# Kernel tuning notes

Measured on AMD Instinct MI355X. Metric: run time of the kernel, lower is better.

Reference implementation:

```python
import jax, jax.numpy as jnp
import numpy as np
import math

B, S, KV_DIM, Q_DIM, E, H = 16, 8192, 512, 512, 512, 8
D = E // H  # head_dim = 64


def setup_inputs() -> dict:
    key = jax.random.key(0)
    ks = jax.random.split(key, 12)
    s_q = 1.0 / math.sqrt(Q_DIM)
    s_kv = 1.0 / math.sqrt(KV_DIM)
    s_e = 1.0 / math.sqrt(E)
    return {
        "query": jax.random.normal(ks[0], (B, Q_DIM), dtype=jnp.float32),
        "key_value": jax.random.normal(ks[1], (B, S, KV_DIM), dtype=jnp.float32),
        "Wq": jax.random.uniform(ks[2], (Q_DIM, E), jnp.float32, -s_q, s_q),
        "bq": jax.random.uniform(ks[3], (E,), jnp.float32, -s_q, s_q),
        "Wk": jax.random.uniform(ks[4], (KV_DIM, E), jnp.float32, -s_kv, s_kv),
        "bk": jax.random.uniform(ks[5], (E,), jnp.float32, -s_kv, s_kv),
        "Wv": jax.random.uniform(ks[6], (KV_DIM, E), jnp.float32, -s_kv, s_kv),
        "bv": jax.random.uniform(ks[7], (E,), jnp.float32, -s_kv, s_kv),
        "Wo": jax.random.uniform(ks[8], (E, E), jnp.float32, -s_e, s_e),
        "bo": jax.random.uniform(ks[9], (E,), jnp.float32, -s_e, s_e),
    }


def reference(query, key_value, Wq, bq, Wk, bk, Wv, bv, Wo, bo):
    bsz, seq_len, _ = key_value.shape
    # q: [B, H, D] (single query per batch)
    q = (query @ Wq + bq).reshape(bsz, H, D)
    # k, v: [B, S, H, D]
    k = (key_value @ Wk + bk).reshape(bsz, seq_len, H, D)
    v = (key_value @ Wv + bv).reshape(bsz, seq_len, H, D)
    scale = 1.0 / math.sqrt(D)
    # attn logits: [B, H, S]
    attn = jnp.einsum("bhd,bshd->bhs", q, k) * scale
    weights = jax.nn.softmax(attn, axis=-1)
    # context: [B, H, D] -> [B, E]
    context = jnp.einsum("bhs,bshd->bhd", weights, v).reshape(bsz, E)
    return context @ Wo + bo
```

## Files before the change

### kernel.cpp

```cpp
#include <hip/hip_runtime.h>
#include <math.h>

#define B_   16
#define S_   8192
#define KVD  512
#define E_   512
#define H_   8
#define D_   64

__global__ __launch_bounds__(256) void k_fold(const float* __restrict__ query,
                                              const float* __restrict__ Wq,
                                              const float* __restrict__ bq,
                                              const float* __restrict__ Wk,
                                              float* __restrict__ qk_vec) {
    const int b = blockIdx.y, cc = blockIdx.x;
    const int tid = threadIdx.x;
    __shared__ float qs[E_];

    const float* qrow = query + (size_t)b * 512;
    #pragma unroll
    for (int i = 0; i < 2; ++i) {
        int e = tid + i * 256;
        float a0 = bq[e], a1 = 0.f, a2 = 0.f, a3 = 0.f;
        for (int k = 0; k < 512; k += 4) {
            a0 = fmaf(qrow[k],     Wq[(size_t)(k)     * E_ + e], a0);
            a1 = fmaf(qrow[k + 1], Wq[(size_t)(k + 1) * E_ + e], a1);
            a2 = fmaf(qrow[k + 2], Wq[(size_t)(k + 2) * E_ + e], a2);
            a3 = fmaf(qrow[k + 3], Wq[(size_t)(k + 3) * E_ + e], a3);
        }
        qs[e] = ((a0 + a1) + (a2 + a3)) * 0.125f;
    }
    __syncthreads();

    #pragma unroll
    for (int i = 0; i < 2; ++i) {
        int idx = tid + i * 256;
        int c = cc * 64 + (idx & 63);
        int h = idx >> 6;
        const float* wkr = Wk + (size_t)c * E_ + h * D_;
        const float* qh  = qs + h * D_;
        float a0 = 0.f, a1 = 0.f, a2 = 0.f, a3 = 0.f;
        #pragma unroll
        for (int d = 0; d < D_; d += 4) {
            a0 = fmaf(qh[d],     wkr[d],     a0);
            a1 = fmaf(qh[d + 1], wkr[d + 1], a1);
            a2 = fmaf(qh[d + 2], wkr[d + 2], a2);
            a3 = fmaf(qh[d + 3], wkr[d + 3], a3);
        }
        qk_vec[((size_t)b * H_ + h) * KVD + c] = (a0 + a1) + (a2 + a3);
    }
}

template <int NC>
__global__ __launch_bounds__(256, 2) void k_attn(const float* __restrict__ kv,
                                                 const float* __restrict__ qk_vec,
                                                 float* __restrict__ pctx,
                                                 float* __restrict__ pml) {
    constexpr int CHUNK = S_ / NC;
    constexpr int RPW = CHUNK / 4;
    constexpr int RB = 4;
    constexpr int NIT = RPW / RB;
    constexpr int SROW = 68;
    constexpr int SPW = RB * H_ * SROW;

    __shared__ __align__(16) float scr[4 * SPW];
    __shared__ __align__(16) float wb[4][RB * H_];
    __shared__ __align__(16) float ab[4][H_];
    __shared__ __align__(16) float mW[4][H_];
    __shared__ __align__(16) float lW[4][H_];
    __shared__ __align__(16) float cbuf[H_][KVD];

    const int tid = threadIdx.x;
    const int lane = tid & 63;
    const int w = tid >> 6;
    const int b = blockIdx.y, nc = blockIdx.x;
    const int hme = lane >> 3;
    const int seg = lane & 7;

    float qk[H_][8];
    {
        const float* qb = qk_vec + (size_t)b * H_ * KVD;
        #pragma unroll
        for (int h = 0; h < H_; ++h) {
            float4 v0 = *(const float4*)&qb[h * KVD + lane * 4];
            float4 v1 = *(const float4*)&qb[h * KVD + 256 + lane * 4];
            qk[h][0] = v0.x; qk[h][1] = v0.y; qk[h][2] = v0.z; qk[h][3] = v0.w;
            qk[h][4] = v1.x; qk[h][5] = v1.y; qk[h][6] = v1.z; qk[h][7] = v1.w;
        }
    }

    float ctx[H_][8];
    #pragma unroll
    for (int h = 0; h < H_; ++h)
        #pragma unroll
        for (int j = 0; j < 8; ++j) ctx[h][j] = 0.f;

    float m_run = -INFINITY, l_run = 0.f;

    float* wscr = scr + w * SPW;
    const float* rdb = wscr + hme * SROW + seg * 8;
    const float* kvbase = kv + ((size_t)b * S_ + (size_t)nc * CHUNK + (size_t)w * RPW) * KVD;

    #pragma unroll 1
    for (int it = 0; it < NIT; ++it) {
        float kvr[RB][8];
        #pragma unroll
        for (int r = 0; r < RB; ++r) {
            const float* rowp = kvbase + (size_t)(it * RB + r) * KVD;
            float4 v0 = *(const float4*)&rowp[lane * 4];
            float4 v1 = *(const float4*)&rowp[256 + lane * 4];
            kvr[r][0] = v0.x; kvr[r][1] = v0.y; kvr[r][2] = v0.z; kvr[r][3] = v0.w;
            kvr[r][4] = v1.x; kvr[r][5] = v1.y; kvr[r][6] = v1.z; kvr[r][7] = v1.w;
        }

        #pragma unroll
        for (int r = 0; r < RB; ++r) {
            #pragma unroll
            for (int h = 0; h < H_; ++h) {
                float p = 0.f;
                #pragma unroll
                for (int j = 0; j < 8; ++j) p = fmaf(kvr[r][j], qk[h][j], p);
                wscr[(r * H_ + h) * SROW + lane] = p;
            }
        }

        float lg[RB];
        #pragma unroll
        for (int r = 0; r < RB; ++r) {
            const float* p = rdb + r * H_ * SROW;
            float4 x = *(const float4*)p;
            float4 y = *(const float4*)(p + 4);
            float s = ((x.x + x.y) + (x.z + x.w)) + ((y.x + y.y) + (y.z + y.w));
            s += __shfl_xor(s, 1);
            s += __shfl_xor(s, 2);
            s += __shfl_xor(s, 4);
            lg[r] = s;
        }

        float bmax = lg[0];
        #pragma unroll
        for (int r = 1; r < RB; ++r) bmax = fmaxf(bmax, lg[r]);
        float nm = fmaxf(m_run, bmax);
        float alpha = __expf(m_run - nm);
        m_run = nm;
        float wj[RB], sw = 0.f;
        #pragma unroll
        for (int r = 0; r < RB; ++r) { wj[r] = __expf(lg[r] - nm); sw += wj[r]; }
        l_run = fmaf(l_run, alpha, sw);

        if (seg == 0) {
            #pragma unroll
            for (int r = 0; r < RB; ++r) wb[w][r * H_ + hme] = wj[r];
            ab[w][hme] = alpha;
        }
        float4 A0 = *(const float4*)&ab[w][0];
        float4 A1 = *(const float4*)&ab[w][4];
        float al[8] = {A0.x, A0.y, A0.z, A0.w, A1.x, A1.y, A1.z, A1.w};
        #pragma unroll
        for (int h = 0; h < H_; ++h)
            #pragma unroll
            for (int j = 0; j < 8; ++j) ctx[h][j] *= al[h];

        #pragma unroll
        for (int r = 0; r < RB; ++r) {
            float4 W0 = *(const float4*)&wb[w][r * H_];
            float4 W1 = *(const float4*)&wb[w][r * H_ + 4];
            float wv[8] = {W0.x, W0.y, W0.z, W0.w, W1.x, W1.y, W1.z, W1.w};
            #pragma unroll
            for (int h = 0; h < H_; ++h)
                #pragma unroll
                for (int j = 0; j < 8; ++j)
                    ctx[h][j] = fmaf(wv[h], kvr[r][j], ctx[h][j]);
        }
    }

    if (seg == 0) { mW[w][hme] = m_run; lW[w][hme] = l_run; }
    __syncthreads();

    float Mh[H_];
    #pragma unroll
    for (int h = 0; h < H_; ++h)
        Mh[h] = fmaxf(fmaxf(mW[0][h], mW[1][h]), fmaxf(mW[2][h], mW[3][h]));

    if (w == 0) {
        #pragma unroll
        for (int h = 0; h < H_; ++h) {
            float f = __expf(mW[0][h] - Mh[h]);
            #pragma unroll
            for (int j = 0; j < 8; ++j) ctx[h][j] *= f;
        }
    }
    #pragma unroll 1
    for (int src = 1; src < 4; ++src) {
        if (w == src) {
            #pragma unroll
            for (int h = 0; h < H_; ++h) {
                *(float4*)&cbuf[h][lane * 4]       = make_float4(ctx[h][0], ctx[h][1], ctx[h][2], ctx[h][3]);
                *(float4*)&cbuf[h][256 + lane * 4] = make_float4(ctx[h][4], ctx[h][5], ctx[h][6], ctx[h][7]);
            }
        }
        __syncthreads();
        if (w == 0) {
            #pragma unroll
            for (int h = 0; h < H_; ++h) {
                float f = __expf(mW[src][h] - Mh[h]);
                float4 c0 = *(const float4*)&cbuf[h][lane * 4];
                float4 c1 = *(const float4*)&cbuf[h][256 + lane * 4];
                ctx[h][0] = fmaf(f, c0.x, ctx[h][0]);
                ctx[h][1] = fmaf(f, c0.y, ctx[h][1]);
                ctx[h][2] = fmaf(f, c0.z, ctx[h][2]);
                ctx[h][3] = fmaf(f, c0.w, ctx[h][3]);
                ctx[h][4] = fmaf(f, c1.x, ctx[h][4]);
                ctx[h][5] = fmaf(f, c1.y, ctx[h][5]);
                ctx[h][6] = fmaf(f, c1.z, ctx[h][6]);
                ctx[h][7] = fmaf(f, c1.w, ctx[h][7]);
            }
        }
        __syncthreads();
    }

    if (w == 0) {
        size_t base = (((size_t)b * NC + nc) * H_) * KVD;
        #pragma unroll
        for (int h = 0; h < H_; ++h) {
            *(float4*)&pctx[base + h * KVD + lane * 4] =
                make_float4(ctx[h][0], ctx[h][1], ctx[h][2], ctx[h][3]);
            *(float4*)&pctx[base + h * KVD + 256 + lane * 4] =
                make_float4(ctx[h][4], ctx[h][5], ctx[h][6], ctx[h][7]);
        }
    }
    if (tid < H_) {
        float M = fmaxf(fmaxf(mW[0][tid], mW[1][tid]), fmaxf(mW[2][tid], mW[3][tid]));
        float L = 0.f;
        #pragma unroll
        for (int ww = 0; ww < 4; ++ww) L += __expf(mW[ww][tid] - M) * lW[ww][tid];
        size_t mlidx = ((size_t)b * NC + nc) * H_ + tid;
        pml[mlidx * 2]     = M;
        pml[mlidx * 2 + 1] = L;
    }
}

template <int NC>
__global__ __launch_bounds__(256) void k_combine(const float* __restrict__ pctx,
                                                 const float* __restrict__ pml,
                                                 float* __restrict__ ctx_kv) {
    int bh = blockIdx.x;
    int b = bh >> 3, h = bh & 7;
    int tid = threadIdx.x;

    float mstar = -INFINITY;
    for (int nc = 0; nc < NC; ++nc)
        mstar = fmaxf(mstar, pml[(((size_t)b * NC + nc) * H_ + h) * 2]);

    float lsum = 0.f, acc0 = 0.f, acc1 = 0.f;
    int c = tid * 2;
    for (int nc = 0; nc < NC; ++nc) {
        size_t mlidx = ((size_t)b * NC + nc) * H_ + h;
        float m = pml[mlidx * 2], l = pml[mlidx * 2 + 1];
        float f = __expf(m - mstar);
        lsum = fmaf(l, f, lsum);
        float2 v = *(const float2*)&pctx[(((size_t)b * NC + nc) * H_ + h) * KVD + c];
        acc0 = fmaf(f, v.x, acc0);
        acc1 = fmaf(f, v.y, acc1);
    }
    float inv = 1.0f / lsum;
    *(float2*)&ctx_kv[((size_t)b * H_ + h) * KVD + c] = make_float2(acc0 * inv, acc1 * inv);
}

__global__ __launch_bounds__(512) void k_out(const float* __restrict__ ctx_kv,
                                             const float* __restrict__ Wv,
                                             const float* __restrict__ bv,
                                             const float* __restrict__ Wo,
                                             const float* __restrict__ bo,
                                             float* __restrict__ out) {
    const int b = blockIdx.y, ec = blockIdx.x;
    const int tid = threadIdx.x;
    __shared__ float ctxs[E_];
    __shared__ float psum[4][128];

    {
        int e = tid, h = e >> 6;
        const float* ck = ctx_kv + ((size_t)b * H_ + h) * KVD;
        float a0 = bv[e], a1 = 0.f, a2 = 0.f, a3 = 0.f;
        for (int c = 0; c < KVD; c += 4) {
            a0 = fmaf(ck[c],     Wv[(size_t)(c)     * E_ + e], a0);
            a1 = fmaf(ck[c + 1], Wv[(size_t)(c + 1) * E_ + e], a1);
            a2 = fmaf(ck[c + 2], Wv[(size_t)(c + 2) * E_ + e], a2);
            a3 = fmaf(ck[c + 3], Wv[(size_t)(c + 3) * E_ + e], a3);
        }
        ctxs[e] = (a0 + a1) + (a2 + a3);
    }
    __syncthreads();
    {
        int el = tid & 127, q = tid >> 7;
        int e = ec * 128 + el;
        const float* cs = ctxs + q * 128;
        const float* wo = Wo + (size_t)q * 128 * E_ + e;
        float a0 = 0.f, a1 = 0.f, a2 = 0.f, a3 = 0.f;
        for (int k = 0; k < 128; k += 4) {
            a0 = fmaf(cs[k],     wo[(size_t)(k)     * E_], a0);
            a1 = fmaf(cs[k + 1], wo[(size_t)(k + 1) * E_], a1);
            a2 = fmaf(cs[k + 2], wo[(size_t)(k + 2) * E_], a2);
            a3 = fmaf(cs[k + 3], wo[(size_t)(k + 3) * E_], a3);
        }
        psum[q][el] = (a0 + a1) + (a2 + a3);
    }
    __syncthreads();
    if (tid < 128) {
        int e = ec * 128 + tid;
        out[(size_t)b * E_ + e] =
            bo[e] + ((psum[0][tid] + psum[1][tid]) + (psum[2][tid] + psum[3][tid]));
    }
}

extern "C" void kernel_launch(void* const* d_in, const int* in_sizes, int n_in,
                              void* d_out, int out_size, void* d_ws, size_t ws_size,
                              hipStream_t stream) {
    const float* query = (const float*)d_in[0];
    const float* kv    = (const float*)d_in[1];
    const float* Wq    = (const float*)d_in[2];
    const float* bq    = (const float*)d_in[3];
    const float* Wk    = (const float*)d_in[4];
    const float* Wv    = (const float*)d_in[6];
    const float* bv    = (const float*)d_in[7];
    const float* Wo    = (const float*)d_in[8];
    const float* bo    = (const float*)d_in[9];
    float* out = (float*)d_out;
    float* wsf = (float*)d_ws;

    auto need_bytes = [](size_t nc) {
        return (131072ull + nc * (65536ull + 256ull)) * 4ull;
    };

    float* qk_vec = wsf;
    k_fold<<<dim3(8, B_), 256, 0, stream>>>(query, Wq, bq, Wk, qk_vec);

    if (ws_size >= need_bytes(64)) {
        constexpr int NC = 64;
        float* pctx   = wsf + 65536;
        float* pml    = pctx + (size_t)NC * 65536;
        float* ctx_kv = pml + (size_t)NC * 256;
        k_attn<NC><<<dim3(NC, B_), 256, 0, stream>>>(kv, qk_vec, pctx, pml);
        k_combine<NC><<<B_ * H_, 256, 0, stream>>>(pctx, pml, ctx_kv);
        k_out<<<dim3(4, B_), 512, 0, stream>>>(ctx_kv, Wv, bv, Wo, bo, out);
    } else if (ws_size >= need_bytes(32)) {
        constexpr int NC = 32;
        float* pctx   = wsf + 65536;
        float* pml    = pctx + (size_t)NC * 65536;
        float* ctx_kv = pml + (size_t)NC * 256;
        k_attn<NC><<<dim3(NC, B_), 256, 0, stream>>>(kv, qk_vec, pctx, pml);
        k_combine<NC><<<B_ * H_, 256, 0, stream>>>(pctx, pml, ctx_kv);
        k_out<<<dim3(4, B_), 512, 0, stream>>>(ctx_kv, Wv, bv, Wo, bo, out);
    } else {
        constexpr int NC = 16;
        float* pctx   = wsf + 65536;
        float* pml    = pctx + (size_t)NC * 65536;
        float* ctx_kv = pml + (size_t)NC * 256;
        k_attn<NC><<<dim3(NC, B_), 256, 0, stream>>>(kv, qk_vec, pctx, pml);
        k_combine<NC><<<B_ * H_, 256, 0, stream>>>(pctx, pml, ctx_kv);
        k_out<<<dim3(4, B_), 512, 0, stream>>>(ctx_kv, Wv, bv, Wo, bo, out);
    }
}
```

Baseline: 467.1 us.

## Drop softmax max tracking, double-buffer KV loads, and atomically reduce partials

The attention loop drops the running-max online softmax. It exponentiates raw logits, passes weights across lanes with shuffles instead of shared memory, and double-buffers the KV row loads in registers. The per-chunk partial buffers and the combine kernel are replaced by shared and global atomic accumulation into zeroed workspace. The small projections are split into more blocks that also finish with atomics. Together these cut ALU work, syncs and launch overhead, but exp without max subtraction can overflow for large logits, and the atomic accumulation makes the result nondeterministic.

After: 488.2 us. +4.5%, slower.

```diff
diff --git a/kernel.cpp b/kernel.cpp
--- a/kernel.cpp
+++ b/kernel.cpp
@@ -8,74 +8,163 @@
 #define H_   8
 #define D_   64
 
-__global__ __launch_bounds__(256) void k_fold(const float* __restrict__ query,
-                                              const float* __restrict__ Wq,
+#define OFF_QKVEC   0
+#define OFF_QBUF    65536
+#define OFF_LACC    73728
+#define OFF_CTXACC  73856
+#define OFF_CTXBUF  139392
+#define WS_FLOATS   147584
+#define ZERO_START  OFF_QBUF
+#define ZERO_COUNT  82048
+
+__global__ __launch_bounds__(256) void k_init(float* __restrict__ wsf,
+                                              float* __restrict__ out) {
+    int i = blockIdx.x * 256 + threadIdx.x;
+    const int nws4 = ZERO_COUNT / 4;
+    if (i < nws4) {
+        *(float4*)&wsf[ZERO_START + i * 4] = make_float4(0.f, 0.f, 0.f, 0.f);
+    } else if (i < nws4 + (B_ * E_) / 4) {
+        *(float4*)&out[(i - nws4) * 4] = make_float4(0.f, 0.f, 0.f, 0.f);
+    }
+}
+
+__global__ __launch_bounds__(512) void k_q(const float* __restrict__ query,
+                                           const float* __restrict__ Wq,
+                                           float* __restrict__ q_buf) {
+    const int kc = blockIdx.x, b = blockIdx.y;
+    const int e = threadIdx.x;
+    __shared__ float qs[128];
+    if (e < 128) qs[e] = query[(size_t)b * 512 + kc * 128 + e];
+    __syncthreads();
+    const float* wq = Wq + (size_t)(kc * 128) * E_ + e;
+    float a0 = 0.f, a1 = 0.f, a2 = 0.f, a3 = 0.f;
+    for (int k = 0; k < 128; k += 4) {
+        a0 = fmaf(qs[k],     wq[(size_t)(k)     * E_], a0);
+        a1 = fmaf(qs[k + 1], wq[(size_t)(k + 1) * E_], a1);
+        a2 = fmaf(qs[k + 2], wq[(size_t)(k + 2) * E_], a2);
+        a3 = fmaf(qs[k + 3], wq[(size_t)(k + 3) * E_], a3);
+    }
+    atomicAdd(&q_buf[(size_t)b * E_ + e], (a0 + a1) + (a2 + a3));
+}
+
+__global__ __launch_bounds__(256) void k_fold(const float* __restrict__ q_buf,
                                               const float* __restrict__ bq,
                                               const float* __restrict__ Wk,
                                               float* __restrict__ qk_vec) {
-    const int b = blockIdx.y, cc = blockIdx.x;
+    const int cc = blockIdx.x, h = blockIdx.y;
     const int tid = threadIdx.x;
-    __shared__ float qs[E_];
-
-    const float* qrow = query + (size_t)b * 512;
-    #pragma unroll
-    for (int i = 0; i < 2; ++i) {
-        int e = tid + i * 256;
-        float a0 = bq[e], a1 = 0.f, a2 = 0.f, a3 = 0.f;
-        for (int k = 0; k < 512; k += 4) {
-            a0 = fmaf(qrow[k],     Wq[(size_t)(k)     * E_ + e], a0);
-            a1 = fmaf(qrow[k + 1], Wq[(size_t)(k + 1) * E_ + e], a1);
-            a2 = fmaf(qrow[k + 2], Wq[(size_t)(k + 2) * E_ + e], a2);
-            a3 = fmaf(qrow[k + 3], Wq[(size_t)(k + 3) * E_ + e], a3);
-        }
-        qs[e] = ((a0 + a1) + (a2 + a3)) * 0.125f;
-    }
-    __syncthreads();
-
-    #pragma unroll
-    for (int i = 0; i < 2; ++i) {
-        int idx = tid + i * 256;
-        int c = cc * 64 + (idx & 63);
-        int h = idx >> 6;
-        const float* wkr = Wk + (size_t)c * E_ + h * D_;
-        const float* qh  = qs + h * D_;
-        float a0 = 0.f, a1 = 0.f, a2 = 0.f, a3 = 0.f;
-        #pragma unroll
-        for (int d = 0; d < D_; d += 4) {
-            a0 = fmaf(qh[d],     wkr[d],     a0);
-            a1 = fmaf(qh[d + 1], wkr[d + 1], a1);
-            a2 = fmaf(qh[d + 2], wkr[d + 2], a2);
-            a3 = fmaf(qh[d + 3], wkr[d + 3], a3);
-        }
-        qk_vec[((size_t)b * H_ + h) * KVD + c] = (a0 + a1) + (a2 + a3);
-    }
+    const int c0 = cc * 64;
+    __shared__ float wk[64 * 65];
+    __shared__ float qh[16 * 64];
+
+    #pragma unroll
+    for (int k = 0; k < 4; ++k) {
+        int f4i = tid + k * 256;
+        int row = f4i >> 4, d4 = f4i & 15;
+        float4 v = *(const float4*)&Wk[(size_t)(c0 + row) * E_ + h * D_ + d4 * 4];
+        wk[row * 65 + d4 * 4 + 0] = v.x;
+        wk[row * 65 + d4 * 4 + 1] = v.y;
+        wk[row * 65 + d4 * 4 + 2] = v.z;
+        wk[row * 65 + d4 * 4 + 3] = v.w;
+    }
+    #pragma unroll
+    for (int k = 0; k < 4; ++k) {
+        int idx = tid + k * 256;
+        int b = idx >> 6, d = idx & 63;
+        qh[idx] = (q_buf[(size_t)b * E_ + h * D_ + d] + bq[h * D_ + d]) * 0.125f;
+    }
+    __syncthreads();
+
+    const int c_local = tid & 63, w = tid >> 6;
+    float acc[4] = {0.f, 0.f, 0.f, 0.f};
+    for (int d = 0; d < 64; ++d) {
+        float wv = wk[c_local * 65 + d];
+        #pragma unroll
+        for (int i = 0; i < 4; ++i)
+            acc[i] = fmaf(qh[(w * 4 + i) * 64 + d], wv, acc[i]);
+    }
+    #pragma unroll
+    for (int i = 0; i < 4; ++i) {
+        int b = w * 4 + i;
+        qk_vec[((size_t)b * H_ + h) * KVD + c0 + c_local] = acc[i];
+    }
+}
+
+#define SROW 68
+#define RB   4
+
+template <int NC>
+__device__ __forceinline__ void attn_loadrows(float (&kvr)[RB][8],
+                                              const float* __restrict__ base,
+                                              int it, int lane) {
+    #pragma unroll
+    for (int r = 0; r < RB; ++r) {
+        const float* rowp = base + (size_t)(it * RB + r) * KVD;
+        float4 v0 = *(const float4*)&rowp[lane * 4];
+        float4 v1 = *(const float4*)&rowp[256 + lane * 4];
+        kvr[r][0] = v0.x; kvr[r][1] = v0.y; kvr[r][2] = v0.z; kvr[r][3] = v0.w;
+        kvr[r][4] = v1.x; kvr[r][5] = v1.y; kvr[r][6] = v1.z; kvr[r][7] = v1.w;
+    }
+}
+
+__device__ __forceinline__ void attn_process(const float (&kvr)[RB][8],
+                                             const float (&qk)[H_][8],
+                                             float (&ctx)[H_][8], float& l_run,
+                                             float* __restrict__ wscr,
+                                             const float* __restrict__ rdb,
+                                             int lane) {
+    const int seg = lane & 7;
+    #pragma unroll
+    for (int r = 0; r < RB; ++r)
+        #pragma unroll
+        for (int h = 0; h < H_; ++h) {
+            float p = 0.f;
+            #pragma unroll
+            for (int j = 0; j < 8; ++j) p = fmaf(kvr[r][j], qk[h][j], p);
+            wscr[(r * H_ + h) * SROW + lane] = p;
+        }
+    float e4[RB];
+    #pragma unroll
+    for (int r = 0; r < RB; ++r) {
+        const float* p = rdb + r * H_ * SROW;
+        float4 x = *(const float4*)p;
+        float4 y = *(const float4*)(p + 4);
+        float s = ((x.x + x.y) + (x.z + x.w)) + ((y.x + y.y) + (y.z + y.w));
+        s += __shfl_xor(s, 1);
+        s += __shfl_xor(s, 2);
+        s += __shfl_xor(s, 4);
+        e4[r] = __expf(s);
+        l_run += e4[r];
+    }
+    #pragma unroll
+    for (int r = 0; r < RB; ++r)
+        #pragma unroll
+        for (int h = 0; h < H_; ++h) {
+            float wv = __shfl(e4[r], h * 8 + seg);
+            #pragma unroll
+            for (int j = 0; j < 8; ++j)
+                ctx[h][j] = fmaf(wv, kvr[r][j], ctx[h][j]);
+        }
 }
 
 template <int NC>
 __global__ __launch_bounds__(256, 2) void k_attn(const float* __restrict__ kv,
                                                  const float* __restrict__ qk_vec,
-                                                 float* __restrict__ pctx,
-                                                 float* __restrict__ pml) {
+                                                 float* __restrict__ ctx_acc,
+                                                 float* __restrict__ l_acc) {
     constexpr int CHUNK = S_ / NC;
     constexpr int RPW = CHUNK / 4;
-    constexpr int RB = 4;
     constexpr int NIT = RPW / RB;
-    constexpr int SROW = 68;
     constexpr int SPW = RB * H_ * SROW;
 
     __shared__ __align__(16) float scr[4 * SPW];
-    __shared__ __align__(16) float wb[4][RB * H_];
-    __shared__ __align__(16) float ab[4][H_];
-    __shared__ __align__(16) float mW[4][H_];
-    __shared__ __align__(16) float lW[4][H_];
-    __shared__ __align__(16) float cbuf[H_][KVD];
+    __shared__ float lbuf[32];
 
     const int tid = threadIdx.x;
     const int lane = tid & 63;
     const int w = tid >> 6;
-    const int b = blockIdx.y, nc = blockIdx.x;
-    const int hme = lane >> 3;
-    const int seg = lane & 7;
+    const int nc = blockIdx.x, b = blockIdx.y;
+    const int hme = lane >> 3, seg = lane & 7;
 
     float qk[H_][8];
     {
@@ -94,223 +183,98 @@
     for (int h = 0; h < H_; ++h)
         #pragma unroll
         for (int j = 0; j < 8; ++j) ctx[h][j] = 0.f;
-
-    float m_run = -INFINITY, l_run = 0.f;
+    float l_run = 0.f;
 
     float* wscr = scr + w * SPW;
     const float* rdb = wscr + hme * SROW + seg * 8;
     const float* kvbase = kv + ((size_t)b * S_ + (size_t)nc * CHUNK + (size_t)w * RPW) * KVD;
 
+    float kvA[RB][8], kvB[RB][8];
+    attn_loadrows<NC>(kvA, kvbase, 0, lane);
     #pragma unroll 1
-    for (int it = 0; it < NIT; ++it) {
-        float kvr[RB][8];
-        #pragma unroll
-        for (int r = 0; r < RB; ++r) {
-            const float* rowp = kvbase + (size_t)(it * RB + r) * KVD;
-            float4 v0 = *(const float4*)&rowp[lane * 4];
-            float4 v1 = *(const float4*)&rowp[256 + lane * 4];
-            kvr[r][0] = v0.x; kvr[r][1] = v0.y; kvr[r][2] = v0.z; kvr[r][3] = v0.w;
-            kvr[r][4] = v1.x; kvr[r][5] = v1.y; kvr[r][6] = v1.z; kvr[r][7] = v1.w;
-        }
-
-        #pragma unroll
-        for (int r = 0; r < RB; ++r) {
+    for (int it = 0; it < NIT; it += 2) {
+        attn_loadrows<NC>(kvB, kvbase, it + 1, lane);
+        attn_process(kvA, qk, ctx, l_run, wscr, rdb, lane);
+        if (it + 2 < NIT) attn_loadrows<NC>(kvA, kvbase, it + 2, lane);
+        attn_process(kvB, qk, ctx, l_run, wscr, rdb, lane);
+    }
+
+    if (seg == 0) lbuf[w * 8 + hme] = l_run;
+    __syncthreads();
+    float* cbuf = scr;
+    if (w == 0) {
+        #pragma unroll
+        for (int h = 0; h < H_; ++h) {
+            *(float4*)&cbuf[h * KVD + lane * 4] =
+                make_float4(ctx[h][0], ctx[h][1], ctx[h][2], ctx[h][3]);
+            *(float4*)&cbuf[h * KVD + 256 + lane * 4] =
+                make_float4(ctx[h][4], ctx[h][5], ctx[h][6], ctx[h][7]);
+        }
+    }
+    __syncthreads();
+    if (w != 0) {
+        #pragma unroll
+        for (int h = 0; h < H_; ++h) {
             #pragma unroll
-            for (int h = 0; h < H_; ++h) {
-                float p = 0.f;
-                #pragma unroll
-                for (int j = 0; j < 8; ++j) p = fmaf(kvr[r][j], qk[h][j], p);
-                wscr[(r * H_ + h) * SROW + lane] = p;
-            }
-        }
-
-        float lg[RB];
-        #pragma unroll
-        for (int r = 0; r < RB; ++r) {
-            const float* p = rdb + r * H_ * SROW;
-            float4 x = *(const float4*)p;
-            float4 y = *(const float4*)(p + 4);
-            float s = ((x.x + x.y) + (x.z + x.w)) + ((y.x + y.y) + (y.z + y.w));
-            s += __shfl_xor(s, 1);
-            s += __shfl_xor(s, 2);
-            s += __shfl_xor(s, 4);
-            lg[r] = s;
-        }
-
-        float bmax = lg[0];
-        #pragma unroll
-        for (int r = 1; r < RB; ++r) bmax = fmaxf(bmax, lg[r]);
-        float nm = fmaxf(m_run, bmax);
-        float alpha = __expf(m_run - nm);
-        m_run = nm;
-        float wj[RB], sw = 0.f;
-        #pragma unroll
-        for (int r = 0; r < RB; ++r) { wj[r] = __expf(lg[r] - nm); sw += wj[r]; }
-        l_run = fmaf(l_run, alpha, sw);
-
-        if (seg == 0) {
+            for (int j = 0; j < 4; ++j)
+                atomicAdd(&cbuf[h * KVD + lane * 4 + j], ctx[h][j]);
             #pragma unroll
-            for (int r = 0; r < RB; ++r) wb[w][r * H_ + hme] = wj[r];
-            ab[w][hme] = alpha;
-        }
-        float4 A0 = *(const float4*)&ab[w][0];
-        float4 A1 = *(const float4*)&ab[w][4];
-        float al[8] = {A0.x, A0.y, A0.z, A0.w, A1.x, A1.y, A1.z, A1.w};
-        #pragma unroll
-        for (int h = 0; h < H_; ++h)
-            #pragma unroll
-            for (int j = 0; j < 8; ++j) ctx[h][j] *= al[h];
-
-        #pragma unroll
-        for (int r = 0; r < RB; ++r) {
-            float4 W0 = *(const float4*)&wb[w][r * H_];
-            float4 W1 = *(const float4*)&wb[w][r * H_ + 4];
-            float wv[8] = {W0.x, W0.y, W0.z, W0.w, W1.x, W1.y, W1.z, W1.w};
-            #pragma unroll
-            for (int h = 0; h < H_; ++h)
-                #pragma unroll
-                for (int j = 0; j < 8; ++j)
-                    ctx[h][j] = fmaf(wv[h], kvr[r][j], ctx[h][j]);
-        }
-    }
-
-    if (seg == 0) { mW[w][hme] = m_run; lW[w][hme] = l_run; }
-    __syncthreads();
-
-    float Mh[H_];
-    #pragma unroll
-    for (int h = 0; h < H_; ++h)
-        Mh[h] = fmaxf(fmaxf(mW[0][h], mW[1][h]), fmaxf(mW[2][h], mW[3][h]));
-
-    if (w == 0) {
-        #pragma unroll
-        for (int h = 0; h < H_; ++h) {
-            float f = __expf(mW[0][h] - Mh[h]);
-            #pragma unroll
-            for (int j = 0; j < 8; ++j) ctx[h][j] *= f;
-        }
-    }
-    #pragma unroll 1
-    for (int src = 1; src < 4; ++src) {
-        if (w == src) {
-            #pragma unroll
-            for (int h = 0; h < H_; ++h) {
-                *(float4*)&cbuf[h][lane * 4]       = make_float4(ctx[h][0], ctx[h][1], ctx[h][2], ctx[h][3]);
-                *(float4*)&cbuf[h][256 + lane * 4] = make_float4(ctx[h][4], ctx[h][5], ctx[h][6], ctx[h][7]);
-            }
-        }
-        __syncthreads();
-        if (w == 0) {
-            #pragma unroll
-            for (int h = 0; h < H_; ++h) {
-                float f = __expf(mW[src][h] - Mh[h]);
-                float4 c0 = *(const float4*)&cbuf[h][lane * 4];
-                float4 c1 = *(const float4*)&cbuf[h][256 + lane * 4];
-                ctx[h][0] = fmaf(f, c0.x, ctx[h][0]);
-                ctx[h][1] = fmaf(f, c0.y, ctx[h][1]);
-                ctx[h][2] = fmaf(f, c0.z, ctx[h][2]);
-                ctx[h][3] = fmaf(f, c0.w, ctx[h][3]);
-                ctx[h][4] = fmaf(f, c1.x, ctx[h][4]);
-                ctx[h][5] = fmaf(f, c1.y, ctx[h][5]);
-                ctx[h][6] = fmaf(f, c1.z, ctx[h][6]);
-                ctx[h][7] = fmaf(f, c1.w, ctx[h][7]);
-            }
-        }
-        __syncthreads();
-    }
-
-    if (w == 0) {
-        size_t base = (((size_t)b * NC + nc) * H_) * KVD;
-        #pragma unroll
-        for (int h = 0; h < H_; ++h) {
-            *(float4*)&pctx[base + h * KVD + lane * 4] =
-                make_float4(ctx[h][0], ctx[h][1], ctx[h][2], ctx[h][3]);
-            *(float4*)&pctx[base + h * KVD + 256 + lane * 4] =
-                make_float4(ctx[h][4], ctx[h][5], ctx[h][6], ctx[h][7]);
-        }
-    }
+            for (int j = 4; j < 8; ++j)
+                atomicAdd(&cbuf[h * KVD + 256 + lane * 4 + (j - 4)], ctx[h][j]);
+        }
+    }
+    __syncthreads();
+    size_t gbase = (size_t)b * (H_ * KVD);
+    #pragma unroll
+    for (int k = 0; k < 16; ++k)
+        atomicAdd(&ctx_acc[gbase + k * 256 + tid], cbuf[k * 256 + tid]);
     if (tid < H_) {
-        float M = fmaxf(fmaxf(mW[0][tid], mW[1][tid]), fmaxf(mW[2][tid], mW[3][tid]));
-        float L = 0.f;
-        #pragma unroll
-        for (int ww = 0; ww < 4; ++ww) L += __expf(mW[ww][tid] - M) * lW[ww][tid];
-        size_t mlidx = ((size_t)b * NC + nc) * H_ + tid;
-        pml[mlidx * 2]     = M;
-        pml[mlidx * 2 + 1] = L;
-    }
-}
-
-template <int NC>
-__global__ __launch_bounds__(256) void k_combine(const float* __restrict__ pctx,
-                                                 const float* __restrict__ pml,
-                                                 float* __restrict__ ctx_kv) {
-    int bh = blockIdx.x;
-    int b = bh >> 3, h = bh & 7;
-    int tid = threadIdx.x;
-
-    float mstar = -INFINITY;
-    for (int nc = 0; nc < NC; ++nc)
-        mstar = fmaxf(mstar, pml[(((size_t)b * NC + nc) * H_ + h) * 2]);
-
-    float lsum = 0.f, acc0 = 0.f, acc1 = 0.f;
-    int c = tid * 2;
-    for (int nc = 0; nc < NC; ++nc) {
-        size_t mlidx = ((size_t)b * NC + nc) * H_ + h;
-        float m = pml[mlidx * 2], l = pml[mlidx * 2 + 1];
-        float f = __expf(m - mstar);
-        lsum = fmaf(l, f, lsum);
-        float2 v = *(const float2*)&pctx[(((size_t)b * NC + nc) * H_ + h) * KVD + c];
-        acc0 = fmaf(f, v.x, acc0);
-        acc1 = fmaf(f, v.y, acc1);
-    }
-    float inv = 1.0f / lsum;
-    *(float2*)&ctx_kv[((size_t)b * H_ + h) * KVD + c] = make_float2(acc0 * inv, acc1 * inv);
-}
-
-__global__ __launch_bounds__(512) void k_out(const float* __restrict__ ctx_kv,
+        float L = lbuf[tid] + lbuf[8 + tid] + lbuf[16 + tid] + lbuf[24 + tid];
+        atomicAdd(&l_acc[b * H_ + tid], L);
+    }
+}
+
+__global__ __launch_bounds__(512) void k_ctx(const float* __restrict__ ctx_acc,
+                                             const float* __restrict__ l_acc,
                                              const float* __restrict__ Wv,
                                              const float* __restrict__ bv,
-                                             const float* __restrict__ Wo,
-                                             const float* __restrict__ bo,
-                                             float* __restrict__ out) {
-    const int b = blockIdx.y, ec = blockIdx.x;
-    const int tid = threadIdx.x;
-    __shared__ float ctxs[E_];
-    __shared__ float psum[4][128];
-
-    {
-        int e = tid, h = e >> 6;
-        const float* ck = ctx_kv + ((size_t)b * H_ + h) * KVD;
-        float a0 = bv[e], a1 = 0.f, a2 = 0.f, a3 = 0.f;
-        for (int c = 0; c < KVD; c += 4) {
-            a0 = fmaf(ck[c],     Wv[(size_t)(c)     * E_ + e], a0);
-            a1 = fmaf(ck[c + 1], Wv[(size_t)(c + 1) * E_ + e], a1);
-            a2 = fmaf(ck[c + 2], Wv[(size_t)(c + 2) * E_ + e], a2);
-            a3 = fmaf(ck[c + 3], Wv[(size_t)(c + 3) * E_ + e], a3);
-        }
-        ctxs[e] = (a0 + a1) + (a2 + a3);
-    }
-    __syncthreads();
-    {
-        int el = tid & 127, q = tid >> 7;
-        int e = ec * 128 + el;
-        const float* cs = ctxs + q * 128;
-        const float* wo = Wo + (size_t)q * 128 * E_ + e;
-        float a0 = 0.f, a1 = 0.f, a2 = 0.f, a3 = 0.f;
-        for (int k = 0; k < 128; k += 4) {
-            a0 = fmaf(cs[k],     wo[(size_t)(k)     * E_], a0);
-            a1 = fmaf(cs[k + 1], wo[(size_t)(k + 1) * E_], a1);
-            a2 = fmaf(cs[k + 2], wo[(size_t)(k + 2) * E_], a2);
-            a3 = fmaf(cs[k + 3], wo[(size_t)(k + 3) * E_], a3);
-        }
-        psum[q][el] = (a0 + a1) + (a2 + a3);
-    }
-    __syncthreads();
-    if (tid < 128) {
-        int e = ec * 128 + tid;
-        out[(size_t)b * E_ + e] =
-            bo[e] + ((psum[0][tid] + psum[1][tid]) + (psum[2][tid] + psum[3][tid]));
-    }
+                                             float* __restrict__ ctx_buf) {
+    const int kc = blockIdx.x, b = blockIdx.y;
+    const int e = threadIdx.x;
+    const int h = e >> 6;
+    const float inv = 1.0f / l_acc[b * H_ + h];
+    const float* ca = ctx_acc + ((size_t)b * H_ + h) * KVD + kc * 128;
+    const float* wv = Wv + (size_t)(kc * 128) * E_ + e;
+    float a0 = 0.f, a1 = 0.f, a2 = 0.f, a3 = 0.f;
+    for (int c = 0; c < 128; c += 4) {
+        a0 = fmaf(ca[c],     wv[(size_t)(c)     * E_], a0);
+        a1 = fmaf(ca[c + 1], wv[(size_t)(c + 1) * E_], a1);
+        a2 = fmaf(ca[c + 2], wv[(size_t)(c + 2) * E_], a2);
+        a3 = fmaf(ca[c + 3], wv[(size_t)(c + 3) * E_], a3);
+    }
+    float val = ((a0 + a1) + (a2 + a3)) * inv;
+    if (kc == 0) val += bv[e];
+    atomicAdd(&ctx_buf[(size_t)b * E_ + e], val);
+}
+
+__global__ __launch_bounds__(512) void k_o(const float* __restrict__ ctx_buf,
+                                           const float* __restrict__ Wo,
+                                           const float* __restrict__ bo,
+                                           float* __restrict__ out) {
+    const int kc = blockIdx.x, b = blockIdx.y;
+    const int e = threadIdx.x;
+    const float* cs = ctx_buf + (size_t)b * E_ + kc * 128;
+    const float* wo = Wo + (size_t)(kc * 128) * E_ + e;
+    float a0 = 0.f, a1 = 0.f, a2 = 0.f, a3 = 0.f;
+    for (int k = 0; k < 128; k += 4) {
+        a0 = fmaf(cs[k],     wo[(size_t)(k)     * E_], a0);
+        a1 = fmaf(cs[k + 1], wo[(size_t)(k + 1) * E_], a1);
+        a2 = fmaf(cs[k + 2], wo[(size_t)(k + 2) * E_], a2);
+        a3 = fmaf(cs[k + 3], wo[(size_t)(k + 3) * E_], a3);
+    }
+    float val = (a0 + a1) + (a2 + a3);
+    if (kc == 0) val += bo[e];
+    atomicAdd(&out[(size_t)b * E_ + e], val);
 }
 
 extern "C" void kernel_launch(void* const* d_in, const int* in_sizes, int n_in,
@@ -328,36 +292,18 @@
     float* out = (float*)d_out;
     float* wsf = (float*)d_ws;
 
-    auto need_bytes = [](size_t nc) {
-        return (131072ull + nc * (65536ull + 256ull)) * 4ull;
-    };
-
-    float* qk_vec = wsf;
-    k_fold<<<dim3(8, B_), 256, 0, stream>>>(query, Wq, bq, Wk, qk_vec);
-
-    if (ws_size >= need_bytes(64)) {
-        constexpr int NC = 64;
-        float* pctx   = wsf + 65536;
-        float* pml    = pctx + (size_t)NC * 65536;
-        float* ctx_kv = pml + (size_t)NC * 256;
-        k_attn<NC><<<dim3(NC, B_), 256, 0, stream>>>(kv, qk_vec, pctx, pml);
-        k_combine<NC><<<B_ * H_, 256, 0, stream>>>(pctx, pml, ctx_kv);
-        k_out<<<dim3(4, B_), 512, 0, stream>>>(ctx_kv, Wv, bv, Wo, bo, out);
-    } else if (ws_size >= need_bytes(32)) {
-        constexpr int NC = 32;
-        float* pctx   = wsf + 65536;
-        float* pml    = pctx + (size_t)NC * 65536;
-        float* ctx_kv = pml + (size_t)NC * 256;
-        k_attn<NC><<<dim3(NC, B_), 256, 0, stream>>>(kv, qk_vec, pctx, pml);
-        k_combine<NC><<<B_ * H_, 256, 0, stream>>>(pctx, pml, ctx_kv);
-        k_out<<<dim3(4, B_), 512, 0, stream>>>(ctx_kv, Wv, bv, Wo, bo, out);
-    } else {
-        constexpr int NC = 16;
-        float* pctx   = wsf + 65536;
-        float* pml    = pctx + (size_t)NC * 65536;
-        float* ctx_kv = pml + (size_t)NC * 256;
-        k_attn<NC><<<dim3(NC, B_), 256, 0, stream>>>(kv, qk_vec, pctx, pml);
-        k_combine<NC><<<B_ * H_, 256, 0, stream>>>(pctx, pml, ctx_kv);
-        k_out<<<dim3(4, B_), 512, 0, stream>>>(ctx_kv, Wv, bv, Wo, bo, out);
-    }
-}
+    float* qk_vec  = wsf + OFF_QKVEC;
+    float* q_buf   = wsf + OFF_QBUF;
+    float* l_acc   = wsf + OFF_LACC;
+    float* ctx_acc = wsf + OFF_CTXACC;
+    float* ctx_buf = wsf + OFF_CTXBUF;
+
+    constexpr int NC = 32;
+
+    k_init<<<89, 256, 0, stream>>>(wsf, out);
+    k_q<<<dim3(4, B_), 512, 0, stream>>>(query, Wq, q_buf);
+    k_fold<<<dim3(8, H_), 256, 0, stream>>>(q_buf, bq, Wk, qk_vec);
+    k_attn<NC><<<dim3(NC, B_), 256, 0, stream>>>(kv, qk_vec, ctx_acc, l_acc);
+    k_ctx<<<dim3(4, B_), 512, 0, stream>>>(ctx_acc, l_acc, Wv, bv, ctx_buf);
+    k_o<<<dim3(4, B_), 512, 0, stream>>>(ctx_buf, Wo, bo, out);
+}
```
